# Kernel tuning notes

Measured on AMD Instinct MI355X. Metric: run time of the kernel, lower is better.

The kernel has to match this reference:

```python
import jax, jax.numpy as jnp
import numpy as np

N = 32768
D = 512          # query_dim = key_dim = value_dim
H = 8            # num_heads


def setup_inputs() -> dict:
    key = jax.random.key(0)
    ks = jax.random.split(key, 8)
    s = 0.02
    return {
        "queries": jax.random.normal(ks[0], (N, D), dtype=jnp.float32),
        "keys": jax.random.normal(ks[1], (N, D), dtype=jnp.float32),
        "values": jax.random.normal(ks[2], (N, D), dtype=jnp.float32),
        # Linear weights stored as [in, out] (torch stores [out, in]; math identical)
        "Wq": jax.random.normal(ks[3], (D, D * H), dtype=jnp.float32) * s,
        "Wk": jax.random.normal(ks[4], (D, D * H), dtype=jnp.float32) * s,
        "Wv": jax.random.normal(ks[5], (D, D * H), dtype=jnp.float32) * s,
        "Wo": jax.random.normal(ks[6], (D * H, D), dtype=jnp.float32) * s,
        "bo": jax.random.normal(ks[7], (D,), dtype=jnp.float32) * s,
    }


def reference(queries, keys, values, Wq, Wk, Wv, Wo, bo):
    # Projections: [N, D] -> [N, H, D]
    Q = (queries @ Wq).reshape(-1, H, D)
    K = (keys @ Wk).reshape(-1, H, D)
    V = (values @ Wv).reshape(-1, H, D)
    # Per-token attention across the HEADS axis (faithful to torch.bmm on [N,H,D])
    attn = jnp.einsum("nhd,ngd->nhg", Q, K)      # [N, H, H], no 1/sqrt(d) scaling
    attn = jax.nn.softmax(attn, axis=-1)
    out = jnp.einsum("nhg,ngd->nhd", attn, V)    # [N, H, D]
    out = out.reshape(-1, H * D)
    return out @ Wo + bo                           # [N, D]
```

## Files before the change

### kernel.cpp

```cpp
#include <hip/hip_runtime.h>
#include <hip/hip_bf16.h>
#include <cstdint>


typedef unsigned short u16;
typedef unsigned int u32;
typedef __bf16 bf16x8 __attribute__((ext_vector_type(8)));
typedef float f32x4 __attribute__((ext_vector_type(4)));

#define DEVI __device__ __forceinline__

DEVI float b2f(u16 u) {
    union { u32 i; float f; } c; c.i = ((u32)u) << 16; return c.f;
}
DEVI u16 f2b(float f) {
    union { float f; u32 i; } c; c.f = f;
    return (u16)((c.i + 0x7FFFu + ((c.i >> 16) & 1u)) >> 16);
}
DEVI float asf(u32 x) { union { u32 i; float f; } c; c.i = x; return c.f; }

DEVI void async16(const u16* g, u16* l) {
    __builtin_amdgcn_global_load_lds(
        (const __attribute__((address_space(1))) u32*)g,
        (__attribute__((address_space(3))) u32*)l, 16, 0, 0);
}


__global__ __launch_bounds__(256) void cvt3_bf16(
    const float* __restrict__ a, const float* __restrict__ b,
    const float* __restrict__ c, u16* __restrict__ out, long ostride) {
    const float* in = (blockIdx.z == 0) ? a : (blockIdx.z == 1) ? b : c;
    u16* o = out + (long)blockIdx.z * ostride;
    const int i = blockIdx.x * 256 + threadIdx.x;
    const float4 x = ((const float4*)in)[2 * i];
    const float4 y = ((const float4*)in)[2 * i + 1];
    union { u16 u[8]; uint4 v; } r;
    r.u[0] = f2b(x.x); r.u[1] = f2b(x.y); r.u[2] = f2b(x.z); r.u[3] = f2b(x.w);
    r.u[4] = f2b(y.x); r.u[5] = f2b(y.y); r.u[6] = f2b(y.z); r.u[7] = f2b(y.w);
    ((uint4*)o)[i] = r.v;
}

__global__ void transpose_cvt(const float* __restrict__ in, u16* __restrict__ out,
                              int R, int C) {
    __shared__ float tile[32][33];
    const int c0 = blockIdx.x * 32, r0 = blockIdx.y * 32;
    const int x = threadIdx.x, y = threadIdx.y;
#pragma unroll
    for (int i = 0; i < 4; ++i) {
        const int r = y + i * 8;
        tile[x][r] = in[(long)(r0 + r) * C + c0 + x];
    }
    __syncthreads();
#pragma unroll
    for (int i = 0; i < 4; ++i) {
        const int c = y + i * 8;
        out[(long)(c0 + c) * R + r0 + x] = f2b(tile[c][x]);
    }
}


#define VM4 asm volatile("s_waitcnt vmcnt(4)" ::: "memory")
#define VM0 asm volatile("s_waitcnt vmcnt(0)" ::: "memory")
#define LGKM0 asm volatile("s_waitcnt lgkmcnt(0)" ::: "memory")
#define NOOP ((void)0)

#define STAGE_A(t, h)                                                     \
    do {                                                                  \
        const u16* _s = pA + (long)(h) * 128 * K + (long)(t) * 64;        \
        u16* _d = As + (((t) & 1) * 16384) + (h) * 8192 + wave * 512;     \
        async16(_s, _d);                                                  \
        async16(_s + 64 * (long)K, _d + 4096);                            \
    } while (0)

#define STAGE_B(t, h)                                                     \
    do {                                                                  \
        const u16* _s = pB + (long)(h) * 128 * K + (long)(t) * 64;        \
        u16* _d = Bs + (((t) & 1) * 16384) + (h) * 8192 + wave * 512;     \
        async16(_s, _d);                                                  \
        async16(_s + 64 * (long)K, _d + 4096);                            \
    } while (0)

#define PHASE(c, P, STG, VW)                                                   \
    {                                                                          \
        const u16* _sA = As + (c) * 16384;                                     \
        const u16* _sB = Bs + (c) * 16384;                                     \
        bf16x8 a00 = *(const bf16x8*)(_sA + arow_u + (2 * (P)) * 1024 + s0);   \
        bf16x8 a01 = *(const bf16x8*)(_sA + arow_u + (2 * (P)) * 1024 + s1);   \
        bf16x8 a10 = *(const bf16x8*)(_sA + arow_u + (2 * (P) + 1) * 1024 + s0); \
        bf16x8 a11 = *(const bf16x8*)(_sA + arow_u + (2 * (P) + 1) * 1024 + s1); \
        if ((P) == 0) {                                                        \
            _Pragma("unroll") for (int n = 0; n < 4; ++n) {                    \
                bfr[n][0] = *(const bf16x8*)(_sB + brow_u + n * 1024 + s0);    \
                bfr[n][1] = *(const bf16x8*)(_sB + brow_u + n * 1024 + s1);    \
            }                                                                  \
        }                                                                      \
        STG;                                                                   \
        __builtin_amdgcn_s_barrier();                                          \
        LGKM0;                                                                 \
        __builtin_amdgcn_s_setprio(1);                                         \
        _Pragma("unroll") for (int n = 0; n < 4; ++n) {                        \
            acc[2 * (P)][n] = __builtin_amdgcn_mfma_f32_16x16x32_bf16(         \
                a00, bfr[n][0], acc[2 * (P)][n], 0, 0, 0);                     \
            acc[2 * (P)][n] = __builtin_amdgcn_mfma_f32_16x16x32_bf16(         \
                a01, bfr[n][1], acc[2 * (P)][n], 0, 0, 0);                     \
            acc[2 * (P) + 1][n] = __builtin_amdgcn_mfma_f32_16x16x32_bf16(     \
                a10, bfr[n][0], acc[2 * (P) + 1][n], 0, 0, 0);                 \
            acc[2 * (P) + 1][n] = __builtin_amdgcn_mfma_f32_16x16x32_bf16(     \
                a11, bfr[n][1], acc[2 * (P) + 1][n], 0, 0, 0);                 \
        }                                                                      \
        __builtin_amdgcn_s_setprio(0);                                         \
        VW;                                                                    \
        __builtin_amdgcn_s_barrier();                                          \
    }

template <int F32OUT>
__global__ __launch_bounds__(512, 2) void gemm256(
    const u16* __restrict__ Ab, const u16* __restrict__ Bb,
    void* __restrict__ Cv, const float* __restrict__ bias,
    int M, int N, int K, long sAz, long sBz, long sCz) {
    __shared__ u16 As[2 * 16384];
    __shared__ u16 Bs[2 * 16384];
    (void)M;
    const int tid = threadIdx.x;
    const int wave = tid >> 6, lane = tid & 63;
    const int z = blockIdx.z;
    const u16* A = Ab + (long)z * sAz;
    const u16* BT = Bb + (long)z * sBz;

    int bx, by;
    {
        const int gx = gridDim.x, nwg = gx * gridDim.y;
        const int b = blockIdx.y * gx + blockIdx.x;
        if ((nwg & 7) == 0) {
            const int cpx = nwg >> 3;
            const int w = (b & 7) * cpx + (b >> 3);
            bx = w % gx; by = w / gx;
        } else { bx = blockIdx.x; by = blockIdx.y; }
    }
    const long row0 = (long)by * 256, col0 = (long)bx * 256;

    const int mrow = lane & 15, quad = lane >> 4;
    const int wr = wave >> 2, wc = wave & 3;
    const int s0 = ((quad ^ (mrow & 7)) << 3);
    const int s1 = (((4 | quad) ^ (mrow & 7)) << 3);
    const int arow_u = (wr * 128 + mrow) * 64;
    const int brow_u = (wc * 64 + mrow) * 64;

    const int sr = tid >> 3;
    const int skg = ((tid & 7) ^ (sr & 7)) << 3;
    const u16* pA = A + (row0 + sr) * (long)K + skg;
    const u16* pB = BT + (col0 + sr) * (long)K + skg;

    f32x4 acc[8][4] = {};
    bf16x8 bfr[4][2];

    const int NT = K >> 6;
    const int NI = NT >> 1;

    STAGE_A(0, 0); STAGE_A(0, 1); STAGE_B(0, 0); STAGE_B(0, 1);
    STAGE_B(1, 0); STAGE_B(1, 1);
    VM4;
    __builtin_amdgcn_s_barrier();

#pragma unroll 1
    for (int it = 0; it < NI - 1; ++it) {
        const int t1 = 2 * it + 1;
        PHASE(0, 0, STAGE_A(t1, 0), NOOP);
        PHASE(0, 1, STAGE_A(t1, 1), NOOP);
        PHASE(0, 2, STAGE_B(t1 + 1, 0), NOOP);
        PHASE(0, 3, STAGE_B(t1 + 1, 1), VM4);
        PHASE(1, 0, STAGE_A(t1 + 1, 0), NOOP);
        PHASE(1, 1, STAGE_A(t1 + 1, 1), NOOP);
        PHASE(1, 2, STAGE_B(t1 + 2, 0), NOOP);
        PHASE(1, 3, STAGE_B(t1 + 2, 1), VM4);
    }
    {
        const int tl = NT - 1;
        PHASE(0, 0, STAGE_A(tl, 0), NOOP);
        PHASE(0, 1, STAGE_A(tl, 1), NOOP);
        PHASE(0, 2, NOOP, NOOP);
        PHASE(0, 3, NOOP, VM0);
        PHASE(1, 0, NOOP, NOOP);
        PHASE(1, 1, NOOP, NOOP);
        PHASE(1, 2, NOOP, NOOP);
        PHASE(1, 3, NOOP, NOOP);
    }

    const long wrow = row0 + wr * 128;
    const long wcol = col0 + wc * 64;
    if (F32OUT) {
        float* C = (float*)Cv + (long)z * sCz;
        float bv[4];
#pragma unroll
        for (int n = 0; n < 4; ++n) bv[n] = bias[wcol + n * 16 + mrow];
#pragma unroll
        for (int m = 0; m < 8; ++m) {
            const long r = wrow + m * 16 + quad * 4;
#pragma unroll
            for (int n = 0; n < 4; ++n) {
                const long c = wcol + n * 16 + mrow;
#pragma unroll
                for (int rr = 0; rr < 4; ++rr)
                    C[(r + rr) * (long)N + c] = acc[m][n][rr] + bv[n];
            }
        }
    } else {
        u16* C = (u16*)Cv + (long)z * sCz;
#pragma unroll
        for (int m = 0; m < 8; ++m) {
            const long r = wrow + m * 16 + quad * 4;
#pragma unroll
            for (int n = 0; n < 4; ++n) {
                const long c = wcol + n * 16 + mrow;
#pragma unroll
                for (int rr = 0; rr < 4; ++rr)
                    C[(r + rr) * (long)N + c] = f2b(acc[m][n][rr]);
            }
        }
    }
}

#undef PHASE
#undef STAGE_A
#undef STAGE_B


DEVI float dot8(uint4 a, uint4 b) {
    const u32* pa = (const u32*)&a;
    const u32* pb = (const u32*)&b;
    float s = 0.f;
#pragma unroll
    for (int w = 0; w < 4; ++w) {
        s = fmaf(asf(pa[w] << 16), asf(pb[w] << 16), s);
        s = fmaf(asf(pa[w] & 0xFFFF0000u), asf(pb[w] & 0xFFFF0000u), s);
    }
    return s;
}

DEVI void acc8(float* o, uint4 v, float p) {
    const u32* pv = (const u32*)&v;
#pragma unroll
    for (int w = 0; w < 4; ++w) {
        o[2 * w]     = fmaf(p, asf(pv[w] << 16), o[2 * w]);
        o[2 * w + 1] = fmaf(p, asf(pv[w] & 0xFFFF0000u), o[2 * w + 1]);
    }
}

__global__ __launch_bounds__(256) void attn_kernel(
    const u16* __restrict__ Qg, const u16* __restrict__ Kg,
    const u16* __restrict__ Vg, u16* __restrict__ Og) {
    __shared__ u16 sQ[4096];
    __shared__ u16 sK[4096];
    __shared__ u16 sV[4096];
    __shared__ float part[4][64];
    __shared__ float probS[64];
    const int t = threadIdx.x;
    const int wave = t >> 6, lane = t & 63;
    const long base = (long)blockIdx.x * 4096;

    {
        const int r0 = wave, r1 = wave + 4;
        async16(Qg + base + r0 * 512 + ((lane ^ r0) << 3), sQ + r0 * 512);
        async16(Qg + base + r1 * 512 + ((lane ^ r1) << 3), sQ + r1 * 512);
        async16(Kg + base + r0 * 512 + ((lane ^ r0) << 3), sK + r0 * 512);
        async16(Kg + base + r1 * 512 + ((lane ^ r1) << 3), sK + r1 * 512);
        async16(Vg + base + r0 * 512 + (lane << 3), sV + r0 * 512);
        async16(Vg + base + r1 * 512 + (lane << 3), sV + r1 * 512);
    }
    __syncthreads();

    {
        const int pr = lane;
        const int h = pr >> 3, g = pr & 7;
        const uint4* q4 = (const uint4*)sQ;
        const uint4* k4 = (const uint4*)sK;
        float s = 0.f;
#pragma unroll
        for (int i = 0; i < 16; ++i) {
            const int c = wave * 16 + i;
            s += dot8(q4[h * 64 + (c ^ h)], k4[g * 64 + (c ^ g)]);
        }
        part[wave][pr] = s;
    }
    __syncthreads();

    if (t < 64) {
        const float sl = part[0][t] + part[1][t] + part[2][t] + part[3][t];
        float m = sl;
        m = fmaxf(m, __shfl_xor(m, 1));
        m = fmaxf(m, __shfl_xor(m, 2));
        m = fmaxf(m, __shfl_xor(m, 4));
        const float e = __expf(sl - m);
        float sum = e;
        sum += __shfl_xor(sum, 1);
        sum += __shfl_xor(sum, 2);
        sum += __shfl_xor(sum, 4);
        probS[t] = e / sum;
    }
    __syncthreads();

    const int hh = t >> 5, c = t & 31;
    const uint4* v4 = (const uint4*)sV;
    float p[8];
#pragma unroll
    for (int g = 0; g < 8; ++g) p[g] = probS[hh * 8 + g];
    float o0[8], o1[8];
#pragma unroll
    for (int j = 0; j < 8; ++j) { o0[j] = 0.f; o1[j] = 0.f; }
#pragma unroll
    for (int g = 0; g < 8; ++g) {
        const uint4 va = v4[g * 64 + c];
        const uint4 vb = v4[g * 64 + 32 + c];
        acc8(o0, va, p[g]);
        acc8(o1, vb, p[g]);
    }
    union { u16 u[8]; uint4 v; } ob;
#pragma unroll
    for (int j = 0; j < 8; ++j) ob.u[j] = f2b(o0[j]);
    *(uint4*)(Og + base + hh * 512 + c * 8) = ob.v;
#pragma unroll
    for (int j = 0; j < 8; ++j) ob.u[j] = f2b(o1[j]);
    *(uint4*)(Og + base + hh * 512 + 256 + c * 8) = ob.v;
}


extern "C" void kernel_launch(void* const* d_in, const int* in_sizes, int n_in,
                              void* d_out, int out_size, void* d_ws, size_t ws_size,
                              hipStream_t stream) {
    const float* Xq = (const float*)d_in[0];
    const float* Xk = (const float*)d_in[1];
    const float* Xv = (const float*)d_in[2];
    const float* Wq = (const float*)d_in[3];
    const float* Wk = (const float*)d_in[4];
    const float* Wv = (const float*)d_in[5];
    const float* Wo = (const float*)d_in[6];
    const float* bo = (const float*)d_in[7];

    const int N = 32768;
    const size_t W = 16777216ull;
    const size_t AO = 268435456ull;

    int McA = 0;
    for (int m = 8192; m >= 1024; m >>= 1)
        if (W + AO + (size_t)m * 27648ull <= ws_size) { McA = m; break; }

    char* ws = (char*)d_ws;
    u16* WqT = (u16*)(ws);
    u16* WoT = (u16*)(ws + 12582912ull);

    dim3 tb(32, 8);
    transpose_cvt<<<dim3(128, 16), tb, 0, stream>>>(Wq, WqT, 512, 4096);
    transpose_cvt<<<dim3(128, 16), tb, 0, stream>>>(Wk, WqT + 2097152, 512, 4096);
    transpose_cvt<<<dim3(128, 16), tb, 0, stream>>>(Wv, WqT + 4194304, 512, 4096);
    transpose_cvt<<<dim3(16, 128), tb, 0, stream>>>(Wo, WoT, 4096, 512);

    if (McA) {
        const int Mc = McA;
        u16* Ao  = (u16*)(ws + W);
        u16* Xb  = (u16*)(ws + W + AO);
        u16* Qc  = Xb + (size_t)3 * Mc * 512;
        u16* Kc  = Qc + (size_t)Mc * 4096;
        u16* Vc  = Kc + (size_t)Mc * 4096;
        const dim3 gProj(16, Mc / 256, 3);
        for (int m0 = 0; m0 < N; m0 += Mc) {
            const long xoff = (long)m0 * 512;
            cvt3_bf16<<<dim3(Mc / 4, 1, 3), 256, 0, stream>>>(
                Xq + xoff, Xk + xoff, Xv + xoff, Xb, (long)Mc * 512);
            gemm256<0><<<gProj, 512, 0, stream>>>(Xb, WqT, Qc, nullptr,
                                                  Mc, 4096, 512,
                                                  (long)Mc * 512, 2097152L,
                                                  (long)Mc * 4096);
            attn_kernel<<<Mc, 256, 0, stream>>>(Qc, Kc, Vc, Ao + (long)m0 * 4096);
        }
        gemm256<1><<<dim3(2, 128, 1), 512, 0, stream>>>(
            Ao, WoT, d_out, bo, N, 512, 4096, 0L, 0L, 0L);
    } else {
        int Mc = 8192;
        while (Mc > 256 && W + (size_t)Mc * 27648ull > ws_size) Mc >>= 1;
        if (W + (size_t)Mc * 27648ull > ws_size) return;
        u16* Xb = (u16*)(ws + W);
        u16* Qc = Xb + (size_t)3 * Mc * 512;
        u16* Kc = Qc + (size_t)Mc * 4096;
        u16* Vc = Kc + (size_t)Mc * 4096;
        const dim3 gProj(16, Mc / 256, 3);
        const dim3 gOut(2, Mc / 256, 1);
        for (int m0 = 0; m0 < N; m0 += Mc) {
            const long xoff = (long)m0 * 512;
            cvt3_bf16<<<dim3(Mc / 4, 1, 3), 256, 0, stream>>>(
                Xq + xoff, Xk + xoff, Xv + xoff, Xb, (long)Mc * 512);
            gemm256<0><<<gProj, 512, 0, stream>>>(Xb, WqT, Qc, nullptr,
                                                  Mc, 4096, 512,
                                                  (long)Mc * 512, 2097152L,
                                                  (long)Mc * 4096);
            attn_kernel<<<Mc, 256, 0, stream>>>(Qc, Kc, Vc, Qc);
            gemm256<1><<<gOut, 512, 0, stream>>>(Qc, WoT, (float*)d_out + xoff, bo,
                                                 Mc, 512, 4096, 0L, 0L, 0L);
        }
    }
}
```

Baseline: 1.370 ms.

## Loop QKV projections inside one persistent GEMM block and vectorize epilogue stores

```diff
diff --git a/kernel.cpp b/kernel.cpp
--- a/kernel.cpp
+++ b/kernel.cpp
@@ -64,17 +64,19 @@
 #define LGKM0 asm volatile("s_waitcnt lgkmcnt(0)" ::: "memory")
 #define NOOP ((void)0)
 
-#define STAGE_A(t, h)                                                     \
+#define STAGE_A(t, h, off)                                                \
     do {                                                                  \
-        const u16* _s = pA + (long)(h) * 128 * K + (long)(t) * 64;        \
+        const u16* _s = Ab + (off) + laneOff + (long)(h) * 128 * K +      \
+                        (long)(t) * 64;                                   \
         u16* _d = As + (((t) & 1) * 16384) + (h) * 8192 + wave * 512;     \
         async16(_s, _d);                                                  \
         async16(_s + 64 * (long)K, _d + 4096);                            \
     } while (0)
 
-#define STAGE_B(t, h)                                                     \
+#define STAGE_B(t, h, off)                                                \
     do {                                                                  \
-        const u16* _s = pB + (long)(h) * 128 * K + (long)(t) * 64;        \
+        const u16* _s = Bb + (off) + laneOff + (long)(h) * 128 * K +      \
+                        (long)(t) * 64;                                   \
         u16* _d = Bs + (((t) & 1) * 16384) + (h) * 8192 + wave * 512;     \
         async16(_s, _d);                                                  \
         async16(_s + 64 * (long)K, _d + 4096);                            \
@@ -100,20 +102,20 @@
         __builtin_amdgcn_s_setprio(1);                                         \
         _Pragma("unroll") for (int n = 0; n < 4; ++n) {                        \
             acc[2 * (P)][n] = __builtin_amdgcn_mfma_f32_16x16x32_bf16(         \
-                a00, bfr[n][0], acc[2 * (P)][n], 0, 0, 0);                     \
+                bfr[n][0], a00, acc[2 * (P)][n], 0, 0, 0);                     \
             acc[2 * (P)][n] = __builtin_amdgcn_mfma_f32_16x16x32_bf16(         \
-                a01, bfr[n][1], acc[2 * (P)][n], 0, 0, 0);                     \
+                bfr[n][1], a01, acc[2 * (P)][n], 0, 0, 0);                     \
             acc[2 * (P) + 1][n] = __builtin_amdgcn_mfma_f32_16x16x32_bf16(     \
-                a10, bfr[n][0], acc[2 * (P) + 1][n], 0, 0, 0);                 \
+                bfr[n][0], a10, acc[2 * (P) + 1][n], 0, 0, 0);                 \
             acc[2 * (P) + 1][n] = __builtin_amdgcn_mfma_f32_16x16x32_bf16(     \
-                a11, bfr[n][1], acc[2 * (P) + 1][n], 0, 0, 0);                 \
+                bfr[n][1], a11, acc[2 * (P) + 1][n], 0, 0, 0);                 \
         }                                                                      \
         __builtin_amdgcn_s_setprio(0);                                         \
         VW;                                                                    \
         __builtin_amdgcn_s_barrier();                                          \
     }
 
-template <int F32OUT>
+template <int F32OUT, int MODE>
 __global__ __launch_bounds__(512, 2) void gemm256(
     const u16* __restrict__ Ab, const u16* __restrict__ Bb,
     void* __restrict__ Cv, const float* __restrict__ bias,
@@ -123,9 +125,6 @@
     (void)M;
     const int tid = threadIdx.x;
     const int wave = tid >> 6, lane = tid & 63;
-    const int z = blockIdx.z;
-    const u16* A = Ab + (long)z * sAz;
-    const u16* BT = Bb + (long)z * sBz;
 
     int bx, by;
     {
@@ -148,76 +147,124 @@
 
     const int sr = tid >> 3;
     const int skg = ((tid & 7) ^ (sr & 7)) << 3;
-    const u16* pA = A + (row0 + sr) * (long)K + skg;
-    const u16* pB = BT + (col0 + sr) * (long)K + skg;
+    const long laneOff = (long)sr * K + skg;
 
     f32x4 acc[8][4] = {};
     bf16x8 bfr[4][2];
 
+    const int NZ = (MODE == 1) ? 3 : 1;
     const int NT = K >> 6;
     const int NI = NT >> 1;
 
-    STAGE_A(0, 0); STAGE_A(0, 1); STAGE_B(0, 0); STAGE_B(0, 1);
-    STAGE_B(1, 0); STAGE_B(1, 1);
+    long oA, oB;
+    if (MODE == 1) {
+        oA = row0 * (long)K;
+        oB = col0 * (long)K;
+    } else {
+        oA = (long)blockIdx.z * sAz + row0 * (long)K;
+        oB = (long)blockIdx.z * sBz + col0 * (long)K;
+    }
+
+    STAGE_A(0, 0, oA); STAGE_A(0, 1, oA);
+    STAGE_B(0, 0, oB); STAGE_B(0, 1, oB);
+    STAGE_B(1, 0, oB); STAGE_B(1, 1, oB);
     VM4;
     __builtin_amdgcn_s_barrier();
 
 #pragma unroll 1
-    for (int it = 0; it < NI - 1; ++it) {
-        const int t1 = 2 * it + 1;
-        PHASE(0, 0, STAGE_A(t1, 0), NOOP);
-        PHASE(0, 1, STAGE_A(t1, 1), NOOP);
-        PHASE(0, 2, STAGE_B(t1 + 1, 0), NOOP);
-        PHASE(0, 3, STAGE_B(t1 + 1, 1), VM4);
-        PHASE(1, 0, STAGE_A(t1 + 1, 0), NOOP);
-        PHASE(1, 1, STAGE_A(t1 + 1, 1), NOOP);
-        PHASE(1, 2, STAGE_B(t1 + 2, 0), NOOP);
-        PHASE(1, 3, STAGE_B(t1 + 2, 1), VM4);
-    }
-    {
-        const int tl = NT - 1;
-        PHASE(0, 0, STAGE_A(tl, 0), NOOP);
-        PHASE(0, 1, STAGE_A(tl, 1), NOOP);
-        PHASE(0, 2, NOOP, NOOP);
-        PHASE(0, 3, NOOP, VM0);
-        PHASE(1, 0, NOOP, NOOP);
-        PHASE(1, 1, NOOP, NOOP);
-        PHASE(1, 2, NOOP, NOOP);
-        PHASE(1, 3, NOOP, NOOP);
-    }
-
-    const long wrow = row0 + wr * 128;
-    const long wcol = col0 + wc * 64;
-    if (F32OUT) {
-        float* C = (float*)Cv + (long)z * sCz;
-        float bv[4];
-#pragma unroll
-        for (int n = 0; n < 4; ++n) bv[n] = bias[wcol + n * 16 + mrow];
-#pragma unroll
-        for (int m = 0; m < 8; ++m) {
-            const long r = wrow + m * 16 + quad * 4;
-#pragma unroll
-            for (int n = 0; n < 4; ++n) {
-                const long c = wcol + n * 16 + mrow;
-#pragma unroll
-                for (int rr = 0; rr < 4; ++rr)
-                    C[(r + rr) * (long)N + c] = acc[m][n][rr] + bv[n];
+    for (int zi = 0; zi < NZ; ++zi) {
+        long oA2, oB2;
+        {
+            const int zn = (zi + 1 < NZ) ? zi + 1 : zi;
+            if (MODE == 1) {
+                oA2 = (long)zn * sAz + row0 * (long)K;
+                oB2 = (long)zn * sBz + col0 * (long)K;
+            } else { oA2 = oA; oB2 = oB; }
+        }
+#pragma unroll 1
+        for (int it = 0; it < NI - 1; ++it) {
+            const int t1 = 2 * it + 1;
+            PHASE(0, 0, STAGE_A(t1, 0, oA), NOOP);
+            PHASE(0, 1, STAGE_A(t1, 1, oA), NOOP);
+            PHASE(0, 2, STAGE_B(t1 + 1, 0, oB), NOOP);
+            PHASE(0, 3, STAGE_B(t1 + 1, 1, oB), VM4);
+            PHASE(1, 0, STAGE_A(t1 + 1, 0, oA), NOOP);
+            PHASE(1, 1, STAGE_A(t1 + 1, 1, oA), NOOP);
+            PHASE(1, 2, STAGE_B(t1 + 2, 0, oB), NOOP);
+            PHASE(1, 3, STAGE_B(t1 + 2, 1, oB), VM4);
+        }
+        if (MODE == 1) {
+            PHASE(0, 0, STAGE_A(NT - 1, 0, oA), NOOP);
+            PHASE(0, 1, STAGE_A(NT - 1, 1, oA), NOOP);
+            PHASE(0, 2, STAGE_B(0, 0, oB2), NOOP);
+            PHASE(0, 3, STAGE_B(0, 1, oB2), VM4);
+            PHASE(1, 0, STAGE_A(0, 0, oA2), NOOP);
+            PHASE(1, 1, STAGE_A(0, 1, oA2), NOOP);
+            PHASE(1, 2, STAGE_B(1, 0, oB2), NOOP);
+            PHASE(1, 3, STAGE_B(1, 1, oB2), VM4);
+        } else {
+            PHASE(0, 0, STAGE_A(NT - 1, 0, oA), NOOP);
+            PHASE(0, 1, STAGE_A(NT - 1, 1, oA), NOOP);
+            PHASE(0, 2, NOOP, NOOP);
+            PHASE(0, 3, NOOP, VM0);
+            PHASE(1, 0, NOOP, NOOP);
+            PHASE(1, 1, NOOP, NOOP);
+            PHASE(1, 2, NOOP, NOOP);
+            PHASE(1, 3, NOOP, NOOP);
+        }
+
+        {
+            const long wrow = row0 + wr * 128;
+            const long wcol = col0 + wc * 64;
+            const long cz = (MODE == 1) ? (long)zi * sCz
+                                        : (long)blockIdx.z * sCz;
+            if (F32OUT) {
+                float* C = (float*)Cv + cz;
+                float4 bv[4];
+#pragma unroll
+                for (int n = 0; n < 4; ++n)
+                    bv[n] = *(const float4*)(bias + wcol + n * 16 + quad * 4);
+#pragma unroll
+                for (int m = 0; m < 8; ++m) {
+                    const long r = wrow + m * 16 + mrow;
+#pragma unroll
+                    for (int n = 0; n < 4; ++n) {
+                        const long c = wcol + n * 16 + quad * 4;
+                        float4 v;
+                        v.x = acc[m][n][0] + bv[n].x;
+                        v.y = acc[m][n][1] + bv[n].y;
+                        v.z = acc[m][n][2] + bv[n].z;
+                        v.w = acc[m][n][3] + bv[n].w;
+                        *(float4*)(C + r * (long)N + c) = v;
+                    }
+                }
+            } else {
+                u16* C = (u16*)Cv + cz;
+#pragma unroll
+                for (int m = 0; m < 8; ++m) {
+                    const long r = wrow + m * 16 + mrow;
+#pragma unroll
+                    for (int n = 0; n < 4; ++n) {
+                        const long c = wcol + n * 16 + quad * 4;
+                        union { u16 u[4]; uint2 v; } ob;
+#pragma unroll
+                        for (int rr = 0; rr < 4; ++rr)
+                            ob.u[rr] = f2b(acc[m][n][rr]);
+                        *(uint2*)(C + r * (long)N + c) = ob.v;
+                    }
+                }
             }
-        }
-    } else {
-        u16* C = (u16*)Cv + (long)z * sCz;
-#pragma unroll
-        for (int m = 0; m < 8; ++m) {
-            const long r = wrow + m * 16 + quad * 4;
-#pragma unroll
-            for (int n = 0; n < 4; ++n) {
-                const long c = wcol + n * 16 + mrow;
-#pragma unroll
-                for (int rr = 0; rr < 4; ++rr)
-                    C[(r + rr) * (long)N + c] = f2b(acc[m][n][rr]);
+            if (zi + 1 < NZ) {
+#pragma unroll
+                for (int m = 0; m < 8; ++m)
+#pragma unroll
+                    for (int n = 0; n < 4; ++n)
+                        acc[m][n] = (f32x4){0.f, 0.f, 0.f, 0.f};
             }
         }
-    }
+        oA = oA2; oB = oB2;
+    }
+    VM0;
 }
 
 #undef PHASE
@@ -361,18 +408,18 @@
         u16* Qc  = Xb + (size_t)3 * Mc * 512;
         u16* Kc  = Qc + (size_t)Mc * 4096;
         u16* Vc  = Kc + (size_t)Mc * 4096;
-        const dim3 gProj(16, Mc / 256, 3);
+        const dim3 gProj(16, Mc / 256, 1);
         for (int m0 = 0; m0 < N; m0 += Mc) {
             const long xoff = (long)m0 * 512;
             cvt3_bf16<<<dim3(Mc / 4, 1, 3), 256, 0, stream>>>(
                 Xq + xoff, Xk + xoff, Xv + xoff, Xb, (long)Mc * 512);
-            gemm256<0><<<gProj, 512, 0, stream>>>(Xb, WqT, Qc, nullptr,
-                                                  Mc, 4096, 512,
-                                                  (long)Mc * 512, 2097152L,
-                                                  (long)Mc * 4096);
+            gemm256<0, 1><<<gProj, 512, 0, stream>>>(Xb, WqT, Qc, nullptr,
+                                                     Mc, 4096, 512,
+                                                     (long)Mc * 512, 2097152L,
+                                                     (long)Mc * 4096);
             attn_kernel<<<Mc, 256, 0, stream>>>(Qc, Kc, Vc, Ao + (long)m0 * 4096);
         }
-        gemm256<1><<<dim3(2, 128, 1), 512, 0, stream>>>(
+        gemm256<1, 0><<<dim3(2, 128, 1), 512, 0, stream>>>(
             Ao, WoT, d_out, bo, N, 512, 4096, 0L, 0L, 0L);
     } else {
         int Mc = 8192;
@@ -382,19 +429,19 @@
         u16* Qc = Xb + (size_t)3 * Mc * 512;
         u16* Kc = Qc + (size_t)Mc * 4096;
         u16* Vc = Kc + (size_t)Mc * 4096;
-        const dim3 gProj(16, Mc / 256, 3);
+        const dim3 gProj(16, Mc / 256, 1);
         const dim3 gOut(2, Mc / 256, 1);
         for (int m0 = 0; m0 < N; m0 += Mc) {
             const long xoff = (long)m0 * 512;
             cvt3_bf16<<<dim3(Mc / 4, 1, 3), 256, 0, stream>>>(
                 Xq + xoff, Xk + xoff, Xv + xoff, Xb, (long)Mc * 512);
-            gemm256<0><<<gProj, 512, 0, stream>>>(Xb, WqT, Qc, nullptr,
-                                                  Mc, 4096, 512,
-                                                  (long)Mc * 512, 2097152L,
-                                                  (long)Mc * 4096);
+            gemm256<0, 1><<<gProj, 512, 0, stream>>>(Xb, WqT, Qc, nullptr,
+                                                     Mc, 4096, 512,
+                                                     (long)Mc * 512, 2097152L,
+                                                     (long)Mc * 4096);
             attn_kernel<<<Mc, 256, 0, stream>>>(Qc, Kc, Vc, Qc);
-            gemm256<1><<<gOut, 512, 0, stream>>>(Qc, WoT, (float*)d_out + xoff, bo,
-                                                 Mc, 512, 4096, 0L, 0L, 0L);
-        }
-    }
-}
+            gemm256<1, 0><<<gOut, 512, 0, stream>>>(Qc, WoT, (float*)d_out + xoff, bo,
+                                                    Mc, 512, 4096, 0L, 0L, 0L);
+        }
+    }
+}
```

Result: slower. 1.457 ms (+6.4%).
